# Optimization experiments

Hardware: AMD Instinct MI355X
Metric: run time of the kernel (lower is better)

Reference implementation:

```python
import jax, jax.numpy as jnp
import numpy as np

V = 4096          # vocab size (blank = V-1)
BLANK = V - 1
D = 512           # encoder dim
J = 640           # joint dim
E = 512           # embedding dim
H = 640           # prediction-net LSTM hidden
T = 8192          # frames


def setup_inputs() -> dict:
    key = jax.random.key(0)
    ks = jax.random.split(key, 12)
    s = lambda *sh: 1.0 / np.sqrt(sh[0])
    return {
        "enc_out": jax.random.normal(ks[0], (1, T, D), jnp.float32),
        "embed":   jax.random.normal(ks[1], (V, E), jnp.float32) * 0.02,
        "Wx":      jax.random.normal(ks[2], (E, 4 * H), jnp.float32) * s(E),
        "Wh":      jax.random.normal(ks[3], (H, 4 * H), jnp.float32) * s(H),
        "b_lstm":  jnp.zeros((4 * H,), jnp.float32),
        "Wdp":     jax.random.normal(ks[4], (H, J), jnp.float32) * s(H),
        "bdp":     jnp.zeros((J,), jnp.float32),
        "Wenc":    jax.random.normal(ks[5], (D, J), jnp.float32) * s(D),
        "benc":    jnp.zeros((J,), jnp.float32),
        "Wout":    jax.random.normal(ks[6], (J, V), jnp.float32) * s(J),
        "bout":    jnp.zeros((V,), jnp.float32),
    }


def _pred_step(tok, h, c, embed, Wx, Wh, b_lstm, Wdp, bdp):
    # single-token LSTM prediction-network step + output projection (decoder.pred)
    e = embed[tok]                                    # [E]
    g = e @ Wx + h @ Wh + b_lstm                      # [4H]
    i, f, gg, o = jnp.split(g, 4)
    c2 = jax.nn.sigmoid(f) * c + jax.nn.sigmoid(i) * jnp.tanh(gg)
    h2 = jax.nn.sigmoid(o) * jnp.tanh(c2)
    dp = h2 @ Wdp + bdp                               # [J] dec projection
    return dp, h2, c2


def reference(enc_out, embed, Wx, Wh, b_lstm, Wdp, bdp, Wenc, benc, Wout, bout):
    # decoder.enc_proj: [1,T,D] -> [T,J]
    enc_proj = enc_out[0] @ Wenc + benc

    # initial pred step fed with the blank token, zero hidden state
    dp0, h0, c0 = _pred_step(BLANK, jnp.zeros((H,), enc_out.dtype),
                             jnp.zeros((H,), enc_out.dtype),
                             embed, Wx, Wh, b_lstm, Wdp, bdp)

    def step(carry, enc_f):
        dp, h, c = carry
        # decoder.joint(enc, dec) = Wout @ tanh(enc_proj + dec_proj), then log_softmax
        logits = jnp.tanh(enc_f + dp) @ Wout + bout   # [V]
        logp = jax.nn.log_softmax(logits, axis=-1)
        tok = jnp.argmax(logp, axis=-1)
        dp2, h2, c2 = _pred_step(tok, h, c, embed, Wx, Wh, b_lstm, Wdp, bdp)
        nb = tok != BLANK                             # advance pred net only on emission
        carry = (jnp.where(nb, dp2, dp), jnp.where(nb, h2, h), jnp.where(nb, c2, c))
        return carry, logp

    _, logps = jax.lax.scan(step, (dp0, h0, c0), enc_proj)  # logps: [T, V]
    return logps
```

## Files before the change

### kernel.cpp

```cpp
#include <hip/hip_runtime.h>
#include <stdint.h>

#define T_FRAMES 8192
#define DIM_D 512
#define DIM_J 640
#define DIM_E 512
#define DIM_H 640
#define DIM_V 4096
#define G4H   2560
#define TOK_BLANK 4095
#define NBLK 256
#define NTHR 256

#define WS_HW   0
#define WS_XW   (WS_HW + 640*8)
#define WS_SA   (WS_XW + 640*8)
#define WS_SB   (WS_SA + 256*8)
#define WS_BAR  (WS_SB + 256*8)

__device__ __forceinline__ float sigm(float x) { return 1.f / (1.f + __expf(-x)); }

__device__ __forceinline__ void st64(unsigned long long* p, unsigned tag, unsigned pay) {
  __hip_atomic_store(p, ((unsigned long long)tag << 32) | (unsigned long long)pay,
                     __ATOMIC_RELAXED, __HIP_MEMORY_SCOPE_AGENT);
}
__device__ __forceinline__ unsigned long long ld64(const unsigned long long* p) {
  return __hip_atomic_load(p, __ATOMIC_RELAXED, __HIP_MEMORY_SCOPE_AGENT);
}
__device__ __forceinline__ bool tagok(unsigned long long w, unsigned tag) {
  return (int)((unsigned)(w >> 32) - tag) >= 0;
}
__device__ __forceinline__ bool tagok16(unsigned long long w, unsigned tag16) {
  return (short)((unsigned short)(w >> 48) - (unsigned short)tag16) >= 0;
}

__device__ __forceinline__ void gbar_init(unsigned* flags, int bid, int tid) {
  __syncthreads();
  if (tid == 0)
    __hip_atomic_store(&flags[bid * 16], 1u, __ATOMIC_RELEASE, __HIP_MEMORY_SCOPE_AGENT);
  unsigned f;
  do { f = __hip_atomic_load(&flags[tid * 16], __ATOMIC_RELAXED, __HIP_MEMORY_SCOPE_AGENT); }
  while ((int)(f - 1u) < 0);
  __builtin_amdgcn_fence(__ATOMIC_ACQUIRE, "agent");
  __syncthreads();
}

extern "C" __global__ void __launch_bounds__(NTHR, 1)
rnnt_greedy3(const float* __restrict__ enc,
             const float* __restrict__ embed,
             const float* __restrict__ Wx,
             const float* __restrict__ Wh,
             const float* __restrict__ b_lstm,
             const float* __restrict__ Wdp,
             const float* __restrict__ bdp,
             const float* __restrict__ Wenc,
             const float* __restrict__ benc,
             const float* __restrict__ Wout,
             const float* __restrict__ bout,
             float* __restrict__ out,
             unsigned long long* __restrict__ hw,
             unsigned long long* __restrict__ xw,
             unsigned long long* __restrict__ sA,
             unsigned long long* __restrict__ sB,
             unsigned* __restrict__ barflag)
{
  __shared__ float smem[28512];

  const int tid  = threadIdx.x;
  const int bid  = blockIdx.x;
  const int wid  = tid >> 6;
  const int lane = tid & 63;

  float* woutl = smem;
  float* wxl   = smem + 10240;
  float* whl   = smem + 16384;
  float* wdpl  = smem + 24064;
  float* h_com = smem + 25984;
  float* h2_l  = smem + 26624;
  float* x_l   = smem + 27264;
  float* ebuf  = smem + 27904;
  float* logit_l = smem + 28416;
  float* g_l     = smem + 28432;
  float* c_l     = smem + 28444;
  float* dpc_l   = smem + 28448;
  float* bout_l  = smem + 28452;
  float* blst_l  = smem + 28468;
  float* bdp_l   = smem + 28480;
  float* red     = smem + 28484;
  float* enc_lds = smem;

  const int h0 = (bid * 5) >> 1;
  const int h1 = ((bid + 1) * 5) >> 1;
  const int nH = h1 - h0;
  const int ncols = nH * 4;
  const int vb = bid << 4;

  {
    const int r0 = bid * 32;
    const float4* src = (const float4*)(enc + (size_t)r0 * DIM_D);
    float4* dst = (float4*)enc_lds;
    for (int i = tid; i < 32 * DIM_D / 4; i += NTHR) dst[i] = src[i];
    __syncthreads();
    for (int jj = tid; jj < DIM_J; jj += NTHR) {
      float acc[32];
      #pragma unroll
      for (int r = 0; r < 32; ++r) acc[r] = 0.f;
      for (int k = 0; k < DIM_D; ++k) {
        float w = Wenc[(size_t)k * DIM_J + jj];
        #pragma unroll
        for (int r = 0; r < 32; ++r) acc[r] += enc_lds[r * DIM_D + k] * w;
      }
      float bj = benc[jj];
      for (int r = 0; r < 32; ++r) out[(size_t)(r0 + r) * DIM_V + jj] = acc[r] + bj;
    }
    __syncthreads();
  }

  for (int idx = tid; idx < 16 * DIM_J; idx += NTHR) {
    int vl = idx / DIM_J, j = idx - vl * DIM_J;
    woutl[idx] = Wout[(size_t)j * DIM_V + vb + vl];
  }
  for (int idx = tid; idx < ncols * DIM_E; idx += NTHR) {
    int c = idx >> 9, k = idx & 511;
    int gcol = (c & 3) * DIM_H + h0 + (c >> 2);
    wxl[idx] = Wx[(size_t)k * G4H + gcol];
  }
  for (int idx = tid; idx < ncols * DIM_H; idx += NTHR) {
    int c = idx / DIM_H, k = idx - c * DIM_H;
    int gcol = (c & 3) * DIM_H + h0 + (c >> 2);
    whl[idx] = Wh[(size_t)k * G4H + gcol];
  }
  for (int idx = tid; idx < nH * DIM_H; idx += NTHR) {
    int jl = idx / DIM_H, k = idx - jl * DIM_H;
    wdpl[idx] = Wdp[(size_t)k * DIM_J + h0 + jl];
  }
  if (tid < 16) bout_l[tid] = bout[vb + tid];
  if (tid < ncols) blst_l[tid] = b_lstm[(tid & 3) * DIM_H + h0 + (tid >> 2)];
  if (tid < nH) bdp_l[tid] = bdp[h0 + tid];
  for (int i = tid; i < DIM_H; i += NTHR) h_com[i] = 0.f;
  if (tid < 4) c_l[tid] = 0.f;

  gbar_init(barflag, bid, tid);

  const int  slot = (wid == 0) ? 0 : wid - 1;
  const int  c0 = slot, c1 = slot + 3, c2 = slot + 6, c3 = slot + 9;
  const bool v2 = (c2 < ncols), v3 = (c3 < ncols);
  const bool lstmw = (wid != 1);

  for (int t = -1; t < T_FRAMES; ++t) {
    const unsigned TAG = (unsigned)(t + 2);
    const bool last = (t == T_FRAMES - 1);

    float encj = 0.f;
    {
      int prow = (t + 1 < T_FRAMES) ? (t + 1) : (T_FRAMES - 1);
      if (wid < nH && lane == 0) encj = out[(size_t)prow * DIM_V + h0 + wid];
    }

    int tok; bool nb;
    if (t >= 0) {
      {
        const float* w0 = woutl + (wid * 4 + 0) * DIM_J;
        const float* w1 = woutl + (wid * 4 + 1) * DIM_J;
        const float* w2 = woutl + (wid * 4 + 2) * DIM_J;
        const float* w3 = woutl + (wid * 4 + 3) * DIM_J;
        float a0 = 0, a1 = 0, a2 = 0, a3 = 0;
        #pragma unroll
        for (int i = 0; i < 10; ++i) {
          int k = lane + (i << 6);
          float xv = x_l[k];
          a0 += xv * w0[k]; a1 += xv * w1[k]; a2 += xv * w2[k]; a3 += xv * w3[k];
        }
        #pragma unroll
        for (int s = 32; s; s >>= 1) {
          a0 += __shfl_xor(a0, s); a1 += __shfl_xor(a1, s);
          a2 += __shfl_xor(a2, s); a3 += __shfl_xor(a3, s);
        }
        if (lane == 0) {
          logit_l[wid * 4 + 0] = a0 + bout_l[wid * 4 + 0];
          logit_l[wid * 4 + 1] = a1 + bout_l[wid * 4 + 1];
          logit_l[wid * 4 + 2] = a2 + bout_l[wid * 4 + 2];
          logit_l[wid * 4 + 3] = a3 + bout_l[wid * 4 + 3];
        }
      }
      __syncthreads();

      if (wid == 0) {
        float v  = (lane < 16) ? logit_l[lane] : -3.4e38f;
        int   vi = vb + (lane & 15);
        float m = v; int mi = vi;
        #pragma unroll
        for (int s = 32; s; s >>= 1) {
          float om = __shfl_xor(m, s); int oi = __shfl_xor(mi, s);
          if (om > m || (om == m && oi < mi)) { m = om; mi = oi; }
        }
        float e = (lane < 16) ? __expf(v) : 0.f;
        #pragma unroll
        for (int s = 32; s; s >>= 1) e += __shfl_xor(e, s);
        if (lane == 0) {
          unsigned long long cw = ((unsigned long long)(TAG & 0xffffu) << 48)
                                | ((unsigned long long)__float_as_uint(m) << 16)
                                | (unsigned long long)(unsigned)(mi & 0xffff);
          __hip_atomic_store(sA + bid, cw, __ATOMIC_RELAXED, __HIP_MEMORY_SCOPE_AGENT);
          st64(sB + bid, TAG, __float_as_uint(e));
        }
        unsigned long long cv0 = 0, cv1 = 0, cv2 = 0, cv3 = 0;
        unsigned rdy = 0;
        while (rdy != 0xfu) {
          if (!(rdy & 1u)) { unsigned long long w = ld64(sA + lane);        if (tagok16(w, TAG)) { cv0 = w; rdy |= 1u; } }
          if (!(rdy & 2u)) { unsigned long long w = ld64(sA + lane + 64);   if (tagok16(w, TAG)) { cv1 = w; rdy |= 2u; } }
          if (!(rdy & 4u)) { unsigned long long w = ld64(sA + lane + 128);  if (tagok16(w, TAG)) { cv2 = w; rdy |= 4u; } }
          if (!(rdy & 8u)) { unsigned long long w = ld64(sA + lane + 192);  if (tagok16(w, TAG)) { cv3 = w; rdy |= 8u; } }
          if (rdy != 0xfu) __builtin_amdgcn_s_sleep(1);
        }
        float bm = -3.4e38f; int bi = 0x7fffffff;
        {
          float mm; int ii;
          mm = __uint_as_float((unsigned)(cv0 >> 16)); ii = ((int)lane << 4)        | (int)(cv0 & 0xfu) | (int)((cv0 >> 4) & 0xff0u);
          ii = (int)(cv0 & 0xffffu);
          if (mm > bm || (mm == bm && ii < bi)) { bm = mm; bi = ii; }
          mm = __uint_as_float((unsigned)(cv1 >> 16)); ii = (int)(cv1 & 0xffffu);
          if (mm > bm || (mm == bm && ii < bi)) { bm = mm; bi = ii; }
          mm = __uint_as_float((unsigned)(cv2 >> 16)); ii = (int)(cv2 & 0xffffu);
          if (mm > bm || (mm == bm && ii < bi)) { bm = mm; bi = ii; }
          mm = __uint_as_float((unsigned)(cv3 >> 16)); ii = (int)(cv3 & 0xffffu);
          if (mm > bm || (mm == bm && ii < bi)) { bm = mm; bi = ii; }
        }
        #pragma unroll
        for (int s = 32; s; s >>= 1) {
          float om = __shfl_xor(bm, s); int oi = __shfl_xor(bi, s);
          if (om > bm || (om == bm && oi < bi)) { bm = om; bi = oi; }
        }
        if (lane == 0) ((int*)red)[0] = bi;
      }
      __syncthreads();
      tok = ((int*)red)[0];
      nb = (tok != TOK_BLANK);
    } else {
      tok = TOK_BLANK; nb = true;
    }

    float4 ev;
    if (wid >= 2 && !last) ev = *(const float4*)(embed + (size_t)tok * DIM_E + (tid - 128) * 4);
    float acc0 = 0, acc1 = 0, acc2 = 0, acc3 = 0;
    if (lstmw && !last) {
      #pragma unroll
      for (int i = 0; i < 10; ++i) {
        int k = lane + (i << 6);
        float hv = h_com[k];
        acc0 += hv * whl[c0 * DIM_H + k];
        acc1 += hv * whl[c1 * DIM_H + k];
        if (v2) acc2 += hv * whl[c2 * DIM_H + k];
        if (v3) acc3 += hv * whl[c3 * DIM_H + k];
      }
    }
    if (wid == 1 && t >= 0) {
      unsigned long long s0 = 0, s1 = 0, s2 = 0, s3 = 0;
      unsigned rdy = 0;
      while (rdy != 0xfu) {
        if (!(rdy & 1u)) { unsigned long long w = ld64(sB + lane);        if (tagok(w, TAG)) { s0 = w; rdy |= 1u; } }
        if (!(rdy & 2u)) { unsigned long long w = ld64(sB + lane + 64);   if (tagok(w, TAG)) { s1 = w; rdy |= 2u; } }
        if (!(rdy & 4u)) { unsigned long long w = ld64(sB + lane + 128);  if (tagok(w, TAG)) { s2 = w; rdy |= 4u; } }
        if (!(rdy & 8u)) { unsigned long long w = ld64(sB + lane + 192);  if (tagok(w, TAG)) { s3 = w; rdy |= 8u; } }
        if (rdy != 0xfu) __builtin_amdgcn_s_sleep(1);
      }
      float s = __uint_as_float((unsigned)s0) + __uint_as_float((unsigned)s1)
              + __uint_as_float((unsigned)s2) + __uint_as_float((unsigned)s3);
      #pragma unroll
      for (int sh = 32; sh; sh >>= 1) s += __shfl_xor(s, sh);
      float lse = __logf(s);
      if (lane < 16) out[(size_t)t * DIM_V + vb + lane] = logit_l[lane] - lse;
    }
    if (wid >= 2 && !last) *(float4*)(ebuf + (tid - 128) * 4) = ev;
    __syncthreads();
    if (last) break;

    if (lstmw) {
      #pragma unroll
      for (int i = 0; i < 8; ++i) {
        int k = lane + (i << 6);
        float evv = ebuf[k];
        acc0 += evv * wxl[c0 * DIM_E + k];
        acc1 += evv * wxl[c1 * DIM_E + k];
        if (v2) acc2 += evv * wxl[c2 * DIM_E + k];
        if (v3) acc3 += evv * wxl[c3 * DIM_E + k];
      }
      #pragma unroll
      for (int s = 32; s; s >>= 1) {
        acc0 += __shfl_xor(acc0, s); acc1 += __shfl_xor(acc1, s);
        acc2 += __shfl_xor(acc2, s); acc3 += __shfl_xor(acc3, s);
      }
      if (lane == 0) {
        g_l[c0] = acc0 + blst_l[c0];
        g_l[c1] = acc1 + blst_l[c1];
        if (v2) g_l[c2] = acc2 + blst_l[c2];
        if (v3) g_l[c3] = acc3 + blst_l[c3];
      }
    }
    __syncthreads();

    if (tid < nH) {
      float c_old = c_l[tid];
      float gi = g_l[tid * 4 + 0], gf = g_l[tid * 4 + 1];
      float gg = g_l[tid * 4 + 2], go_ = g_l[tid * 4 + 3];
      float c2v = sigm(gf) * c_old + sigm(gi) * tanhf(gg);
      float h2v = sigm(go_) * tanhf(c2v);
      c_l[tid] = nb ? c2v : c_old;
      st64(hw + h0 + tid, TAG, __float_as_uint(h2v));
    }
    if (wid == 0) {
      unsigned long long hv[10]; unsigned rdy = 0;
      while (rdy != 0x3ffu) {
        #pragma unroll
        for (int i = 0; i < 10; ++i) {
          if (!(rdy & (1u << i))) {
            unsigned long long w = ld64(hw + lane + (i << 6));
            if (tagok(w, TAG)) { hv[i] = w; rdy |= 1u << i; }
          }
        }
        if (rdy != 0x3ffu) __builtin_amdgcn_s_sleep(1);
      }
      #pragma unroll
      for (int i = 0; i < 10; ++i) {
        int k = lane + (i << 6);
        float h2v = __uint_as_float((unsigned)hv[i]);
        h2_l[k] = h2v;
        h_com[k] = nb ? h2v : h_com[k];
      }
    }
    __syncthreads();

    if (wid < nH) {
      const float* wp = wdpl + wid * DIM_H;
      float a = 0.f;
      #pragma unroll
      for (int i = 0; i < 10; ++i) { int k = lane + (i << 6); a += h2_l[k] * wp[k]; }
      #pragma unroll
      for (int s = 32; s; s >>= 1) a += __shfl_xor(a, s);
      if (lane == 0) {
        float dp2 = a + bdp_l[wid];
        float dpn = nb ? dp2 : dpc_l[wid];
        dpc_l[wid] = dpn;
        st64(xw + h0 + wid, TAG, __float_as_uint(tanhf(encj + dpn)));
      }
    }
    if (wid == 0) {
      unsigned long long xv[10]; unsigned rdy = 0;
      while (rdy != 0x3ffu) {
        #pragma unroll
        for (int i = 0; i < 10; ++i) {
          if (!(rdy & (1u << i))) {
            unsigned long long w = ld64(xw + lane + (i << 6));
            if (tagok(w, TAG)) { xv[i] = w; rdy |= 1u << i; }
          }
        }
        if (rdy != 0x3ffu) __builtin_amdgcn_s_sleep(1);
      }
      #pragma unroll
      for (int i = 0; i < 10; ++i)
        x_l[lane + (i << 6)] = __uint_as_float((unsigned)xv[i]);
    }
    __syncthreads();
  }
}

extern "C" void kernel_launch(void* const* d_in, const int* in_sizes, int n_in,
                              void* d_out, int out_size, void* d_ws, size_t ws_size,
                              hipStream_t stream) {
  const float* enc    = (const float*)d_in[0];
  const float* embed  = (const float*)d_in[1];
  const float* Wx     = (const float*)d_in[2];
  const float* Wh     = (const float*)d_in[3];
  const float* b_lstm = (const float*)d_in[4];
  const float* Wdp    = (const float*)d_in[5];
  const float* bdp    = (const float*)d_in[6];
  const float* Wenc   = (const float*)d_in[7];
  const float* benc   = (const float*)d_in[8];
  const float* Wout   = (const float*)d_in[9];
  const float* bout   = (const float*)d_in[10];
  float* out = (float*)d_out;
  char* ws = (char*)d_ws;
  unsigned long long* hw = (unsigned long long*)(ws + WS_HW);
  unsigned long long* xw = (unsigned long long*)(ws + WS_XW);
  unsigned long long* sA = (unsigned long long*)(ws + WS_SA);
  unsigned long long* sB = (unsigned long long*)(ws + WS_SB);
  unsigned* barflag = (unsigned*)(ws + WS_BAR);

  hipLaunchKernelGGL(rnnt_greedy3, dim3(NBLK), dim3(NTHR), 0, stream,
                     enc, embed, Wx, Wh, b_lstm, Wdp, bdp, Wenc, benc, Wout, bout,
                     out, hw, xw, sA, sB, barflag);
}
```

Baseline: 129.4 ms.

## Route cross-block reductions through a hub block with replicated broadcast flags

Block 0 becomes a hub: it alone polls all 256 blocks' argmax and exp-sum partials and all h/x slices, then publishes the token, log-sum-exp and epoch flags to 8 replicated slots. Other blocks poll a single word instead of scanning every peer's slot. The Wh matvec is reassigned to warps 2-3 and overlapped with the token wait, while warp 1 handles the softmax normaliser and enc prefetch concurrently. This cuts global polling traffic but adds one extra hop of latency through the hub on every step.

```diff
diff --git a/kernel.cpp b/kernel.cpp
--- a/kernel.cpp
+++ b/kernel.cpp
@@ -16,7 +16,11 @@
 #define WS_XW   (WS_HW + 640*8)
 #define WS_SA   (WS_XW + 640*8)
 #define WS_SB   (WS_SA + 256*8)
-#define WS_BAR  (WS_SB + 256*8)
+#define WS_TOK  (WS_SB + 256*8)
+#define WS_LSE  (WS_TOK + 64*8)
+#define WS_HEP  (WS_LSE + 64*8)
+#define WS_XEP  (WS_HEP + 64*8)
+#define WS_BAR  (WS_XEP + 64*8)
 
 __device__ __forceinline__ float sigm(float x) { return 1.f / (1.f + __expf(-x)); }
 
@@ -30,8 +34,16 @@
 __device__ __forceinline__ bool tagok(unsigned long long w, unsigned tag) {
   return (int)((unsigned)(w >> 32) - tag) >= 0;
 }
-__device__ __forceinline__ bool tagok16(unsigned long long w, unsigned tag16) {
-  return (short)((unsigned short)(w >> 48) - (unsigned short)tag16) >= 0;
+__device__ __forceinline__ bool tagok16(unsigned long long w, unsigned tag) {
+  return (short)((unsigned short)(w >> 48) - (unsigned short)tag) >= 0;
+}
+__device__ __forceinline__ unsigned long long poll1(const unsigned long long* p, unsigned tag) {
+  unsigned long long w;
+  for (;;) {
+    w = ld64(p);
+    if (tagok(w, tag)) return w;
+    __builtin_amdgcn_s_sleep(1);
+  }
 }
 
 __device__ __forceinline__ void gbar_init(unsigned* flags, int bid, int tid) {
@@ -46,7 +58,7 @@
 }
 
 extern "C" __global__ void __launch_bounds__(NTHR, 1)
-rnnt_greedy3(const float* __restrict__ enc,
+rnnt_greedy4(const float* __restrict__ enc,
              const float* __restrict__ embed,
              const float* __restrict__ Wx,
              const float* __restrict__ Wh,
@@ -62,6 +74,10 @@
              unsigned long long* __restrict__ xw,
              unsigned long long* __restrict__ sA,
              unsigned long long* __restrict__ sB,
+             unsigned long long* __restrict__ tokw,
+             unsigned long long* __restrict__ lsew,
+             unsigned long long* __restrict__ hep,
+             unsigned long long* __restrict__ xep,
              unsigned* __restrict__ barflag)
 {
   __shared__ float smem[28512];
@@ -94,6 +110,7 @@
   const int nH = h1 - h0;
   const int ncols = nH * 4;
   const int vb = bid << 4;
+  const bool hub = (bid == 0);
 
   {
     const int r0 = bid * 32;
@@ -139,53 +156,46 @@
   if (tid < nH) bdp_l[tid] = bdp[h0 + tid];
   for (int i = tid; i < DIM_H; i += NTHR) h_com[i] = 0.f;
   if (tid < 4) c_l[tid] = 0.f;
+  if (tid < 16) red[tid] = 0.f;
 
   gbar_init(barflag, bid, tid);
 
-  const int  slot = (wid == 0) ? 0 : wid - 1;
-  const int  c0 = slot, c1 = slot + 3, c2 = slot + 6, c3 = slot + 9;
-  const bool v2 = (c2 < ncols), v3 = (c3 < ncols);
-  const bool lstmw = (wid != 1);
+  const int cbase = (wid >= 2) ? (wid - 2) : 0;
 
   for (int t = -1; t < T_FRAMES; ++t) {
     const unsigned TAG = (unsigned)(t + 2);
     const bool last = (t == T_FRAMES - 1);
 
-    float encj = 0.f;
-    {
-      int prow = (t + 1 < T_FRAMES) ? (t + 1) : (T_FRAMES - 1);
-      if (wid < nH && lane == 0) encj = out[(size_t)prow * DIM_V + h0 + wid];
-    }
-
-    int tok; bool nb;
     if (t >= 0) {
-      {
-        const float* w0 = woutl + (wid * 4 + 0) * DIM_J;
-        const float* w1 = woutl + (wid * 4 + 1) * DIM_J;
-        const float* w2 = woutl + (wid * 4 + 2) * DIM_J;
-        const float* w3 = woutl + (wid * 4 + 3) * DIM_J;
-        float a0 = 0, a1 = 0, a2 = 0, a3 = 0;
-        #pragma unroll
-        for (int i = 0; i < 10; ++i) {
-          int k = lane + (i << 6);
-          float xv = x_l[k];
-          a0 += xv * w0[k]; a1 += xv * w1[k]; a2 += xv * w2[k]; a3 += xv * w3[k];
-        }
-        #pragma unroll
-        for (int s = 32; s; s >>= 1) {
-          a0 += __shfl_xor(a0, s); a1 += __shfl_xor(a1, s);
-          a2 += __shfl_xor(a2, s); a3 += __shfl_xor(a3, s);
-        }
-        if (lane == 0) {
-          logit_l[wid * 4 + 0] = a0 + bout_l[wid * 4 + 0];
-          logit_l[wid * 4 + 1] = a1 + bout_l[wid * 4 + 1];
-          logit_l[wid * 4 + 2] = a2 + bout_l[wid * 4 + 2];
-          logit_l[wid * 4 + 3] = a3 + bout_l[wid * 4 + 3];
-        }
-      }
-      __syncthreads();
-
-      if (wid == 0) {
+      const float* w0 = woutl + (wid * 4 + 0) * DIM_J;
+      const float* w1 = woutl + (wid * 4 + 1) * DIM_J;
+      const float* w2 = woutl + (wid * 4 + 2) * DIM_J;
+      const float* w3 = woutl + (wid * 4 + 3) * DIM_J;
+      float a0 = 0, a1 = 0, a2 = 0, a3 = 0;
+      #pragma unroll
+      for (int i = 0; i < 10; ++i) {
+        int k = lane + (i << 6);
+        float xv = x_l[k];
+        a0 += xv * w0[k]; a1 += xv * w1[k]; a2 += xv * w2[k]; a3 += xv * w3[k];
+      }
+      #pragma unroll
+      for (int s = 32; s; s >>= 1) {
+        a0 += __shfl_xor(a0, s); a1 += __shfl_xor(a1, s);
+        a2 += __shfl_xor(a2, s); a3 += __shfl_xor(a3, s);
+      }
+      if (lane == 0) {
+        logit_l[wid * 4 + 0] = a0 + bout_l[wid * 4 + 0];
+        logit_l[wid * 4 + 1] = a1 + bout_l[wid * 4 + 1];
+        logit_l[wid * 4 + 2] = a2 + bout_l[wid * 4 + 2];
+        logit_l[wid * 4 + 3] = a3 + bout_l[wid * 4 + 3];
+      }
+    }
+    __syncthreads();
+
+    float whacc[6] = {0, 0, 0, 0, 0, 0};
+
+    if (wid == 0) {
+      if (t >= 0 && !last) {
         float v  = (lane < 16) ? logit_l[lane] : -3.4e38f;
         int   vi = vb + (lane & 15);
         float m = v; int mi = vi;
@@ -194,138 +204,179 @@
           float om = __shfl_xor(m, s); int oi = __shfl_xor(mi, s);
           if (om > m || (om == m && oi < mi)) { m = om; mi = oi; }
         }
-        float e = (lane < 16) ? __expf(v) : 0.f;
-        #pragma unroll
-        for (int s = 32; s; s >>= 1) e += __shfl_xor(e, s);
         if (lane == 0) {
           unsigned long long cw = ((unsigned long long)(TAG & 0xffffu) << 48)
                                 | ((unsigned long long)__float_as_uint(m) << 16)
                                 | (unsigned long long)(unsigned)(mi & 0xffff);
           __hip_atomic_store(sA + bid, cw, __ATOMIC_RELAXED, __HIP_MEMORY_SCOPE_AGENT);
-          st64(sB + bid, TAG, __float_as_uint(e));
-        }
-        unsigned long long cv0 = 0, cv1 = 0, cv2 = 0, cv3 = 0;
-        unsigned rdy = 0;
-        while (rdy != 0xfu) {
-          if (!(rdy & 1u)) { unsigned long long w = ld64(sA + lane);        if (tagok16(w, TAG)) { cv0 = w; rdy |= 1u; } }
-          if (!(rdy & 2u)) { unsigned long long w = ld64(sA + lane + 64);   if (tagok16(w, TAG)) { cv1 = w; rdy |= 2u; } }
-          if (!(rdy & 4u)) { unsigned long long w = ld64(sA + lane + 128);  if (tagok16(w, TAG)) { cv2 = w; rdy |= 4u; } }
-          if (!(rdy & 8u)) { unsigned long long w = ld64(sA + lane + 192);  if (tagok16(w, TAG)) { cv3 = w; rdy |= 8u; } }
-          if (rdy != 0xfu) __builtin_amdgcn_s_sleep(1);
-        }
-        float bm = -3.4e38f; int bi = 0x7fffffff;
-        {
-          float mm; int ii;
-          mm = __uint_as_float((unsigned)(cv0 >> 16)); ii = ((int)lane << 4)        | (int)(cv0 & 0xfu) | (int)((cv0 >> 4) & 0xff0u);
-          ii = (int)(cv0 & 0xffffu);
-          if (mm > bm || (mm == bm && ii < bi)) { bm = mm; bi = ii; }
-          mm = __uint_as_float((unsigned)(cv1 >> 16)); ii = (int)(cv1 & 0xffffu);
-          if (mm > bm || (mm == bm && ii < bi)) { bm = mm; bi = ii; }
-          mm = __uint_as_float((unsigned)(cv2 >> 16)); ii = (int)(cv2 & 0xffffu);
-          if (mm > bm || (mm == bm && ii < bi)) { bm = mm; bi = ii; }
-          mm = __uint_as_float((unsigned)(cv3 >> 16)); ii = (int)(cv3 & 0xffffu);
-          if (mm > bm || (mm == bm && ii < bi)) { bm = mm; bi = ii; }
-        }
-        #pragma unroll
-        for (int s = 32; s; s >>= 1) {
-          float om = __shfl_xor(bm, s); int oi = __shfl_xor(bi, s);
-          if (om > bm || (om == bm && oi < bi)) { bm = om; bi = oi; }
-        }
-        if (lane == 0) ((int*)red)[0] = bi;
-      }
-      __syncthreads();
-      tok = ((int*)red)[0];
-      nb = (tok != TOK_BLANK);
+        }
+        int tokv;
+        if (hub) {
+          unsigned long long w0v = 0, w1v = 0, w2v = 0, w3v = 0;
+          unsigned rdy = 0;
+          while (rdy != 0xfu) {
+            if (!(rdy & 1u)) { unsigned long long w = ld64(sA + lane);        if (tagok16(w, TAG)) { w0v = w; rdy |= 1u; } }
+            if (!(rdy & 2u)) { unsigned long long w = ld64(sA + lane + 64);   if (tagok16(w, TAG)) { w1v = w; rdy |= 2u; } }
+            if (!(rdy & 4u)) { unsigned long long w = ld64(sA + lane + 128);  if (tagok16(w, TAG)) { w2v = w; rdy |= 4u; } }
+            if (!(rdy & 8u)) { unsigned long long w = ld64(sA + lane + 192);  if (tagok16(w, TAG)) { w3v = w; rdy |= 8u; } }
+            if (rdy != 0xfu) __builtin_amdgcn_s_sleep(1);
+          }
+          float bm = -3.4e38f; int bi = 0x7fffffff;
+          {
+            float mm; int ii;
+            mm = __uint_as_float((unsigned)(w0v >> 16)); ii = (int)(w0v & 0xffffu);
+            if (mm > bm || (mm == bm && ii < bi)) { bm = mm; bi = ii; }
+            mm = __uint_as_float((unsigned)(w1v >> 16)); ii = (int)(w1v & 0xffffu);
+            if (mm > bm || (mm == bm && ii < bi)) { bm = mm; bi = ii; }
+            mm = __uint_as_float((unsigned)(w2v >> 16)); ii = (int)(w2v & 0xffffu);
+            if (mm > bm || (mm == bm && ii < bi)) { bm = mm; bi = ii; }
+            mm = __uint_as_float((unsigned)(w3v >> 16)); ii = (int)(w3v & 0xffffu);
+            if (mm > bm || (mm == bm && ii < bi)) { bm = mm; bi = ii; }
+          }
+          #pragma unroll
+          for (int s = 32; s; s >>= 1) {
+            float om = __shfl_xor(bm, s); int oi = __shfl_xor(bi, s);
+            if (om > bm || (om == bm && oi < bi)) { bm = om; bi = oi; }
+          }
+          if (lane < 8) st64(tokw + lane * 8, TAG, (unsigned)bi);
+          tokv = bi;
+        } else {
+          unsigned long long w = 0;
+          if (lane == 0) w = poll1(tokw + (bid & 7) * 8, TAG);
+          w = __shfl(w, 0);
+          tokv = (int)(unsigned)(w & 0xffffffffu);
+        }
+        if (lane == 0)
+          ((volatile int*)red)[0] = (int)(((TAG & 0xffffu) << 16) | (unsigned)tokv);
+      }
+    } else if (wid == 1) {
+      if (t >= 0) {
+        float e = (lane < 16) ? __expf(logit_l[lane]) : 0.f;
+        #pragma unroll
+        for (int s = 32; s; s >>= 1) e += __shfl_xor(e, s);
+        if (lane == 0) st64(sB + bid, TAG, __float_as_uint(e));
+        float lse;
+        if (hub) {
+          unsigned long long s0 = 0, s1 = 0, s2 = 0, s3 = 0;
+          unsigned rdy = 0;
+          while (rdy != 0xfu) {
+            if (!(rdy & 1u)) { unsigned long long w = ld64(sB + lane);        if (tagok(w, TAG)) { s0 = w; rdy |= 1u; } }
+            if (!(rdy & 2u)) { unsigned long long w = ld64(sB + lane + 64);   if (tagok(w, TAG)) { s1 = w; rdy |= 2u; } }
+            if (!(rdy & 4u)) { unsigned long long w = ld64(sB + lane + 128);  if (tagok(w, TAG)) { s2 = w; rdy |= 4u; } }
+            if (!(rdy & 8u)) { unsigned long long w = ld64(sB + lane + 192);  if (tagok(w, TAG)) { s3 = w; rdy |= 8u; } }
+            if (rdy != 0xfu) __builtin_amdgcn_s_sleep(1);
+          }
+          float s = __uint_as_float((unsigned)s0) + __uint_as_float((unsigned)s1)
+                  + __uint_as_float((unsigned)s2) + __uint_as_float((unsigned)s3);
+          #pragma unroll
+          for (int sh = 32; sh; sh >>= 1) s += __shfl_xor(s, sh);
+          lse = __logf(s);
+          if (lane < 8) st64(lsew + lane * 8, TAG, __float_as_uint(lse));
+        } else {
+          unsigned long long w = 0;
+          if (lane == 0) w = poll1(lsew + (bid & 7) * 8, TAG);
+          w = __shfl(w, 0);
+          lse = __uint_as_float((unsigned)(w & 0xffffffffu));
+        }
+        if (lane < 16) out[(size_t)t * DIM_V + vb + lane] = logit_l[lane] - lse;
+      }
+      if (!last && lane < nH) {
+        int prow = t + 1;
+        red[8 + lane] = out[(size_t)prow * DIM_V + h0 + lane];
+      }
     } else {
-      tok = TOK_BLANK; nb = true;
-    }
-
-    float4 ev;
-    if (wid >= 2 && !last) ev = *(const float4*)(embed + (size_t)tok * DIM_E + (tid - 128) * 4);
-    float acc0 = 0, acc1 = 0, acc2 = 0, acc3 = 0;
-    if (lstmw && !last) {
-      #pragma unroll
-      for (int i = 0; i < 10; ++i) {
-        int k = lane + (i << 6);
-        float hv = h_com[k];
-        acc0 += hv * whl[c0 * DIM_H + k];
-        acc1 += hv * whl[c1 * DIM_H + k];
-        if (v2) acc2 += hv * whl[c2 * DIM_H + k];
-        if (v3) acc3 += hv * whl[c3 * DIM_H + k];
-      }
-    }
-    if (wid == 1 && t >= 0) {
-      unsigned long long s0 = 0, s1 = 0, s2 = 0, s3 = 0;
-      unsigned rdy = 0;
-      while (rdy != 0xfu) {
-        if (!(rdy & 1u)) { unsigned long long w = ld64(sB + lane);        if (tagok(w, TAG)) { s0 = w; rdy |= 1u; } }
-        if (!(rdy & 2u)) { unsigned long long w = ld64(sB + lane + 64);   if (tagok(w, TAG)) { s1 = w; rdy |= 2u; } }
-        if (!(rdy & 4u)) { unsigned long long w = ld64(sB + lane + 128);  if (tagok(w, TAG)) { s2 = w; rdy |= 4u; } }
-        if (!(rdy & 8u)) { unsigned long long w = ld64(sB + lane + 192);  if (tagok(w, TAG)) { s3 = w; rdy |= 8u; } }
-        if (rdy != 0xfu) __builtin_amdgcn_s_sleep(1);
-      }
-      float s = __uint_as_float((unsigned)s0) + __uint_as_float((unsigned)s1)
-              + __uint_as_float((unsigned)s2) + __uint_as_float((unsigned)s3);
-      #pragma unroll
-      for (int sh = 32; sh; sh >>= 1) s += __shfl_xor(s, sh);
-      float lse = __logf(s);
-      if (lane < 16) out[(size_t)t * DIM_V + vb + lane] = logit_l[lane] - lse;
-    }
-    if (wid >= 2 && !last) *(float4*)(ebuf + (tid - 128) * 4) = ev;
+      if (!last) {
+        #pragma unroll
+        for (int ci = 0; ci < 6; ++ci) {
+          int c = cbase + ci * 2;
+          if (c < ncols) {
+            const float* wh = whl + c * DIM_H;
+            float a = 0.f;
+            #pragma unroll
+            for (int i = 0; i < 10; ++i) { int k = lane + (i << 6); a += h_com[k] * wh[k]; }
+            whacc[ci] = a;
+          }
+        }
+        int tokv = TOK_BLANK;
+        if (t >= 0) {
+          volatile int* rp = (volatile int*)red;
+          int v;
+          for (;;) {
+            v = rp[0];
+            if (((unsigned)v >> 16) == (TAG & 0xffffu)) break;
+            __builtin_amdgcn_s_sleep(1);
+          }
+          tokv = v & 0xffff;
+        }
+        float4 ev = *(const float4*)(embed + (size_t)tokv * DIM_E + (tid - 128) * 4);
+        *(float4*)(ebuf + (tid - 128) * 4) = ev;
+      }
+    }
     __syncthreads();
     if (last) break;
 
-    if (lstmw) {
-      #pragma unroll
-      for (int i = 0; i < 8; ++i) {
-        int k = lane + (i << 6);
-        float evv = ebuf[k];
-        acc0 += evv * wxl[c0 * DIM_E + k];
-        acc1 += evv * wxl[c1 * DIM_E + k];
-        if (v2) acc2 += evv * wxl[c2 * DIM_E + k];
-        if (v3) acc3 += evv * wxl[c3 * DIM_E + k];
-      }
-      #pragma unroll
-      for (int s = 32; s; s >>= 1) {
-        acc0 += __shfl_xor(acc0, s); acc1 += __shfl_xor(acc1, s);
-        acc2 += __shfl_xor(acc2, s); acc3 += __shfl_xor(acc3, s);
-      }
-      if (lane == 0) {
-        g_l[c0] = acc0 + blst_l[c0];
-        g_l[c1] = acc1 + blst_l[c1];
-        if (v2) g_l[c2] = acc2 + blst_l[c2];
-        if (v3) g_l[c3] = acc3 + blst_l[c3];
-      }
-    }
-    __syncthreads();
-
-    if (tid < nH) {
-      float c_old = c_l[tid];
-      float gi = g_l[tid * 4 + 0], gf = g_l[tid * 4 + 1];
-      float gg = g_l[tid * 4 + 2], go_ = g_l[tid * 4 + 3];
+    int tok = TOK_BLANK;
+    if (t >= 0) tok = ((volatile int*)red)[0] & 0xffff;
+    const bool nb = (t < 0) || (tok != TOK_BLANK);
+
+    if (wid >= 2) {
+      #pragma unroll
+      for (int ci = 0; ci < 6; ++ci) {
+        int c = cbase + ci * 2;
+        if (c < ncols) {
+          const float* wx = wxl + c * DIM_E;
+          float a = whacc[ci];
+          #pragma unroll
+          for (int i = 0; i < 8; ++i) { int k = lane + (i << 6); a += ebuf[k] * wx[k]; }
+          #pragma unroll
+          for (int s = 32; s; s >>= 1) a += __shfl_xor(a, s);
+          if (lane == 0) g_l[c] = a + blst_l[c];
+        }
+      }
+    }
+    __syncthreads();
+
+    if (wid == 2 && lane < nH) {
+      float c_old = c_l[lane];
+      float gi = g_l[lane * 4 + 0], gf = g_l[lane * 4 + 1];
+      float gg = g_l[lane * 4 + 2], go_ = g_l[lane * 4 + 3];
       float c2v = sigm(gf) * c_old + sigm(gi) * tanhf(gg);
       float h2v = sigm(go_) * tanhf(c2v);
-      c_l[tid] = nb ? c2v : c_old;
-      st64(hw + h0 + tid, TAG, __float_as_uint(h2v));
+      c_l[lane] = nb ? c2v : c_old;
+      st64(hw + h0 + lane, TAG, __float_as_uint(h2v));
     }
     if (wid == 0) {
-      unsigned long long hv[10]; unsigned rdy = 0;
-      while (rdy != 0x3ffu) {
+      if (hub) {
+        unsigned long long hv[10]; unsigned rdy = 0;
+        while (rdy != 0x3ffu) {
+          #pragma unroll
+          for (int i = 0; i < 10; ++i) {
+            if (!(rdy & (1u << i))) {
+              unsigned long long w = ld64(hw + lane + (i << 6));
+              if (tagok(w, TAG)) { hv[i] = w; rdy |= 1u << i; }
+            }
+          }
+          if (rdy != 0x3ffu) __builtin_amdgcn_s_sleep(1);
+        }
+        asm volatile("" ::: "memory");
+        if (lane < 8) st64(hep + lane * 8, TAG, 0u);
         #pragma unroll
         for (int i = 0; i < 10; ++i) {
-          if (!(rdy & (1u << i))) {
-            unsigned long long w = ld64(hw + lane + (i << 6));
-            if (tagok(w, TAG)) { hv[i] = w; rdy |= 1u << i; }
-          }
-        }
-        if (rdy != 0x3ffu) __builtin_amdgcn_s_sleep(1);
-      }
-      #pragma unroll
-      for (int i = 0; i < 10; ++i) {
-        int k = lane + (i << 6);
-        float h2v = __uint_as_float((unsigned)hv[i]);
-        h2_l[k] = h2v;
-        h_com[k] = nb ? h2v : h_com[k];
+          int k = lane + (i << 6);
+          float h2v = __uint_as_float((unsigned)hv[i]);
+          h2_l[k] = h2v;
+          h_com[k] = nb ? h2v : h_com[k];
+        }
+      } else {
+        if (lane == 0) (void)poll1(hep + (bid & 7) * 8, TAG);
+        asm volatile("" ::: "memory");
+        #pragma unroll
+        for (int i = 0; i < 10; ++i) {
+          int k = lane + (i << 6);
+          float h2v = __uint_as_float((unsigned)ld64(hw + k));
+          h2_l[k] = h2v;
+          h_com[k] = nb ? h2v : h_com[k];
+        }
       }
     }
     __syncthreads();
@@ -341,24 +392,36 @@
         float dp2 = a + bdp_l[wid];
         float dpn = nb ? dp2 : dpc_l[wid];
         dpc_l[wid] = dpn;
-        st64(xw + h0 + wid, TAG, __float_as_uint(tanhf(encj + dpn)));
+        st64(xw + h0 + wid, TAG, __float_as_uint(tanhf(red[8 + wid] + dpn)));
       }
     }
     if (wid == 0) {
-      unsigned long long xv[10]; unsigned rdy = 0;
-      while (rdy != 0x3ffu) {
+      if (hub) {
+        unsigned long long xv[10]; unsigned rdy = 0;
+        while (rdy != 0x3ffu) {
+          #pragma unroll
+          for (int i = 0; i < 10; ++i) {
+            if (!(rdy & (1u << i))) {
+              unsigned long long w = ld64(xw + lane + (i << 6));
+              if (tagok(w, TAG)) { xv[i] = w; rdy |= 1u << i; }
+            }
+          }
+          if (rdy != 0x3ffu) __builtin_amdgcn_s_sleep(1);
+        }
+        asm volatile("" ::: "memory");
+        if (lane < 8) st64(xep + lane * 8, TAG, 0u);
+        #pragma unroll
+        for (int i = 0; i < 10; ++i)
+          x_l[lane + (i << 6)] = __uint_as_float((unsigned)xv[i]);
+      } else {
+        if (lane == 0) (void)poll1(xep + (bid & 7) * 8, TAG);
+        asm volatile("" ::: "memory");
         #pragma unroll
         for (int i = 0; i < 10; ++i) {
-          if (!(rdy & (1u << i))) {
-            unsigned long long w = ld64(xw + lane + (i << 6));
-            if (tagok(w, TAG)) { xv[i] = w; rdy |= 1u << i; }
-          }
-        }
-        if (rdy != 0x3ffu) __builtin_amdgcn_s_sleep(1);
-      }
-      #pragma unroll
-      for (int i = 0; i < 10; ++i)
-        x_l[lane + (i << 6)] = __uint_as_float((unsigned)xv[i]);
+          int k = lane + (i << 6);
+          x_l[k] = __uint_as_float((unsigned)ld64(xw + k));
+        }
+      }
     }
     __syncthreads();
   }
@@ -380,13 +443,17 @@
   const float* bout   = (const float*)d_in[10];
   float* out = (float*)d_out;
   char* ws = (char*)d_ws;
-  unsigned long long* hw = (unsigned long long*)(ws + WS_HW);
-  unsigned long long* xw = (unsigned long long*)(ws + WS_XW);
-  unsigned long long* sA = (unsigned long long*)(ws + WS_SA);
-  unsigned long long* sB = (unsigned long long*)(ws + WS_SB);
+  unsigned long long* hw   = (unsigned long long*)(ws + WS_HW);
+  unsigned long long* xw   = (unsigned long long*)(ws + WS_XW);
+  unsigned long long* sA   = (unsigned long long*)(ws + WS_SA);
+  unsigned long long* sB   = (unsigned long long*)(ws + WS_SB);
+  unsigned long long* tokw = (unsigned long long*)(ws + WS_TOK);
+  unsigned long long* lsew = (unsigned long long*)(ws + WS_LSE);
+  unsigned long long* hep  = (unsigned long long*)(ws + WS_HEP);
+  unsigned long long* xep  = (unsigned long long*)(ws + WS_XEP);
   unsigned* barflag = (unsigned*)(ws + WS_BAR);
 
-  hipLaunchKernelGGL(rnnt_greedy3, dim3(NBLK), dim3(NTHR), 0, stream,
+  hipLaunchKernelGGL(rnnt_greedy4, dim3(NBLK), dim3(NTHR), 0, stream,
                      enc, embed, Wx, Wh, b_lstm, Wdp, bdp, Wenc, benc, Wout, bout,
-                     out, hw, xw, sA, sB, barflag);
-}
+                     out, hw, xw, sA, sB, tokw, lsew, hep, xep, barflag);
+}
```

Result: slower. 158.1 ms (+22.2%).
